# Kernel tuning notes

Measured on AMD Instinct MI355X. Metric: run time of the kernel, lower is better.

Reference implementation:

```python
import jax, jax.numpy as jnp
import numpy as np

STATE_DIM = 128
EDGE_DIM = 32
INNER_DIM = 256
B, N = 32, 128


def _lin_params(key, fan_in, fan_out):
    kw, kb = jax.random.split(key)
    bound = 1.0 / np.sqrt(fan_in)
    W = jax.random.uniform(kw, (fan_in, fan_out), minval=-bound, maxval=bound, dtype=jnp.float32)
    b = jax.random.uniform(kb, (fan_out,), minval=-bound, maxval=bound, dtype=jnp.float32)
    return W, b


def setup_inputs() -> dict:
    key = jax.random.key(0)
    ks = jax.random.split(key, 10)
    h = jax.random.normal(ks[0], (B, N, STATE_DIM), dtype=jnp.float32)
    edge_feat = jax.random.normal(ks[1], (B, N, N, EDGE_DIM), dtype=jnp.float32)
    edge_mask = jax.random.uniform(ks[2], (B, N, N), dtype=jnp.float32)
    in_dim = 2 * STATE_DIM + EDGE_DIM
    Wm1, bm1 = _lin_params(ks[3], in_dim, INNER_DIM)
    Wm2, bm2 = _lin_params(ks[4], INNER_DIM, STATE_DIM)
    Wg1, bg1 = _lin_params(ks[5], in_dim, INNER_DIM)
    Wg2, bg2 = _lin_params(ks[6], INNER_DIM, 1)
    Wu1, bu1 = _lin_params(ks[7], 2 * STATE_DIM + 1, INNER_DIM)
    Wu2, bu2 = _lin_params(ks[8], INNER_DIM, STATE_DIM)
    ln_w = jnp.ones((STATE_DIM,), jnp.float32)
    ln_b = jnp.zeros((STATE_DIM,), jnp.float32)
    return dict(h=h, edge_feat=edge_feat, edge_mask=edge_mask,
                Wm1=Wm1, bm1=bm1, Wm2=Wm2, bm2=bm2,
                Wg1=Wg1, bg1=bg1, Wg2=Wg2, bg2=bg2,
                Wu1=Wu1, bu1=bu1, Wu2=Wu2, bu2=bu2,
                ln_w=ln_w, ln_b=ln_b)


def _layernorm(x, w, b, eps=1e-5):
    mu = jnp.mean(x, axis=-1, keepdims=True)
    var = jnp.mean((x - mu) ** 2, axis=-1, keepdims=True)
    return (x - mu) * jax.lax.rsqrt(var + eps) * w + b


def reference(h, edge_feat, edge_mask,
              Wm1, bm1, Wm2, bm2,
              Wg1, bg1, Wg2, bg2,
              Wu1, bu1, Wu2, bu2,
              ln_w, ln_b):
    n = h.shape[1]
    # all-pairs concat [B,N,N,2*state+edge]; h_i broadcast over axis 2, h_j over axis 1
    h_i = jnp.broadcast_to(h[:, :, None, :], (h.shape[0], n, n, h.shape[-1]))
    h_j = jnp.broadcast_to(h[:, None, :, :], (h.shape[0], n, n, h.shape[-1]))
    pair = jnp.concatenate([h_i, h_j, edge_feat], axis=-1)
    gate = jax.nn.sigmoid(jnp.tanh(pair @ Wg1 + bg1) @ Wg2 + bg2) * edge_mask[..., None]
    msg = jnp.tanh(pair @ Wm1 + bm1) @ Wm2 + bm2
    denom = jnp.maximum(jnp.sum(gate, axis=2), 1.0)  # [B,N,1]
    agg = jnp.sum(gate * msg, axis=2) / denom  # [B,N,state]
    degree = jnp.sum(edge_mask, axis=-1, keepdims=True)
    degree_norm = degree / max(n - 1, 1)
    upd_in = jnp.concatenate([h, agg, degree_norm], axis=-1)
    delta = jnp.tanh(jnp.tanh(upd_in @ Wu1 + bu1) @ Wu2 + bu2)
    return _layernorm(h + delta, ln_w, ln_b)
```

## Files before the change

### kernel.cpp

```cpp
#include <hip/hip_runtime.h>
#include <hip/hip_bf16.h>

#define BB 32
#define NN 128
#define SD 128
#define ED 32
#define ID 256
#define BN (BB*NN)
#define NI 4

#define WM2B 288
#define WU1B 352
#define WU2B 480

typedef __attribute__((ext_vector_type(8))) short sh8;
typedef __attribute__((ext_vector_type(4))) float f32x4;

__device__ __forceinline__ float ftanh(float x) {
    float e2 = __expf(2.0f * x);
    return 1.0f - 2.0f * __builtin_amdgcn_rcpf(e2 + 1.0f);
}

__device__ __forceinline__ ushort f2bf(float f) {
    unsigned u = __float_as_uint(f);
    return (ushort)((u + 0x7FFF + ((u >> 16) & 1)) >> 16);
}

__device__ __forceinline__ sh8 afragT(const float* base, int stride, int kt, int lane) {
    sh8 v = (sh8){0, 0, 0, 0, 0, 0, 0, 0};
    if ((lane & 15) < 4) {
        const float* p = base + (lane & 15) * stride + kt * 32 + (lane >> 4) * 8;
        f32x4 a0 = *(const f32x4*)p;
        f32x4 a1 = *(const f32x4*)(p + 4);
        v[0] = (short)f2bf(a0[0]); v[1] = (short)f2bf(a0[1]);
        v[2] = (short)f2bf(a0[2]); v[3] = (short)f2bf(a0[3]);
        v[4] = (short)f2bf(a1[0]); v[5] = (short)f2bf(a1[1]);
        v[6] = (short)f2bf(a1[2]); v[7] = (short)f2bf(a1[3]);
    }
    return v;
}

__global__ void k_prep(const float* __restrict__ Wg1, const float* __restrict__ Wm1,
                       const float* __restrict__ Wm2, const float* __restrict__ Wu1,
                       const float* __restrict__ Wu2, ushort* __restrict__ Bprep) {
    const int tt = blockIdx.x;
    const int l = threadIdx.x;
    const float* W;
    int rowbase, nt, stride;
    if (tt < 256) {
        const int tgt = tt >> 6;
        const int kt = (tt >> 4) & 3;
        nt = tt & 15;
        W = (tgt >= 2) ? Wm1 : Wg1;
        rowbase = (tgt & 1) * 128 + kt * 32;
        stride = ID;
    } else if (tt < WM2B) {
        const int wt = tt - 256;
        W = (wt >> 4) ? Wm1 : Wg1;
        rowbase = 2 * SD;
        nt = wt & 15;
        stride = ID;
    } else if (tt < WU1B) {
        const int wt = tt - WM2B;
        W = Wm2; rowbase = (wt >> 3) * 32; nt = wt & 7; stride = SD;
    } else if (tt < WU2B) {
        const int wt = tt - WU1B;
        W = Wu1; rowbase = (wt >> 4) * 32; nt = wt & 15; stride = ID;
    } else {
        const int wt = tt - WU2B;
        W = Wu2; rowbase = (wt >> 3) * 32; nt = wt & 7; stride = SD;
    }
    const int colw = nt * 16 + (l & 15);
    const int kb = rowbase + (l >> 4) * 8;
    sh8 v;
    #pragma unroll
    for (int e = 0; e < 8; ++e)
        v[e] = (short)f2bf(W[(size_t)(kb + e) * stride + colw]);
    *(sh8*)&Bprep[(size_t)tt * 512 + l * 8] = v;
}

__global__ __launch_bounds__(256) void k1_mfma(
        const float* __restrict__ h,
        const float* __restrict__ bg1, const float* __restrict__ bm1,
        const ushort* __restrict__ Bprep,
        float* __restrict__ Hgi, float* __restrict__ Hgjt,
        float* __restrict__ Hmi, float* __restrict__ Hmjt) {
    const int blk = blockIdx.x;
    const int tgt = blockIdx.y;
    const int t = threadIdx.x;
    const int w = t >> 6;
    const int lane = t & 63;
    const int col = lane & 15;
    const int grp = lane >> 4;
    __shared__ __align__(16) ushort Alds[4 * 512];

    {
        const int c = t;
        const int kt = c >> 6, l = c & 63;
        const int row = l & 15;
        const int kb = kt * 32 + (l >> 4) * 8;
        const float* p = h + (size_t)(blk * 16 + row) * SD + kb;
        f32x4 a0 = *(const f32x4*)p;
        f32x4 a1 = *(const f32x4*)(p + 4);
        sh8 v;
        v[0] = (short)f2bf(a0[0]); v[1] = (short)f2bf(a0[1]);
        v[2] = (short)f2bf(a0[2]); v[3] = (short)f2bf(a0[3]);
        v[4] = (short)f2bf(a1[0]); v[5] = (short)f2bf(a1[1]);
        v[6] = (short)f2bf(a1[2]); v[7] = (short)f2bf(a1[3]);
        *(sh8*)&Alds[c * 8] = v;
    }
    __syncthreads();

    const int kcol = w * 64 + col;
    sh8 Af[4];
    #pragma unroll
    for (int kt = 0; kt < 4; ++kt)
        Af[kt] = *(const sh8*)&Alds[kt * 512 + lane * 8];

    f32x4 acc[4];
    #pragma unroll
    for (int n = 0; n < 4; ++n) acc[n] = (f32x4){0.f, 0.f, 0.f, 0.f};
    #pragma unroll
    for (int kt = 0; kt < 4; ++kt)
        #pragma unroll
        for (int n = 0; n < 4; ++n) {
            sh8 Bf = *(const sh8*)&Bprep[
                (size_t)(tgt * 64 + kt * 16 + w * 4 + n) * 512 + lane * 8];
            acc[n] = __builtin_amdgcn_mfma_f32_16x16x32_bf16(
                Af[kt], Bf, acc[n], 0, 0, 0);
        }
    if (tgt & 1) {
        float* out = (tgt == 1) ? Hgjt : Hmjt;
        #pragma unroll
        for (int n = 0; n < 4; ++n)
            *(f32x4*)&out[((size_t)blk * ID + kcol + n * 16) * 16 + grp * 4] = acc[n];
    } else {
        const float* bias = (tgt == 0) ? bg1 : bm1;
        float* out = (tgt == 0) ? Hgi : Hmi;
        #pragma unroll
        for (int n = 0; n < 4; ++n) {
            const float bv = bias[kcol + n * 16];
            #pragma unroll
            for (int r = 0; r < 4; ++r)
                out[(size_t)(blk * 16 + grp * 4 + r) * ID + kcol + n * 16] =
                    acc[n][r] + bv;
        }
    }
}

__global__ __launch_bounds__(256, 4) void k2_fused(
        const float* __restrict__ ef, const float* __restrict__ em,
        const ushort* __restrict__ Bprep,
        const float* __restrict__ Hgi, const float* __restrict__ Hmi,
        const float* __restrict__ Hgjt, const float* __restrict__ Hmjt,
        const float* __restrict__ Wg2, const float* __restrict__ bg2,
        const float* __restrict__ h,
        const float* __restrict__ Wu1, const float* __restrict__ bu1,
        const float* __restrict__ bu2, const float* __restrict__ bm2,
        const float* __restrict__ lnw, const float* __restrict__ lnb,
        float* __restrict__ out) {
    const int bi0 = blockIdx.x * NI;
    const int b = bi0 >> 7;
    const int t = threadIdx.x;
    const int w = t >> 6;
    const int lane = t & 63;
    const int col = lane & 15;
    const int grp = lane >> 4;

    __shared__ __align__(16) ushort Elds[NI * 4 * 512];
    __shared__ float glds[NI][NN];
    __shared__ float gsumL[NI], degL[NI];

    {
        float* gl = &glds[0][0];
        gl[t] = 0.f;
        gl[t + 256] = 0.f;
    }

    const int kcol = w * 64 + col;
    const float* HgjL = Hgjt + (size_t)b * 8 * ID * 16 + (size_t)kcol * 16 + grp * 4;
    const float* HmjL = Hmjt + (size_t)b * 8 * ID * 16 + (size_t)kcol * 16 + grp * 4;
    const float bg2v = bg2[0];

    float ts[NI][4];
    #pragma unroll
    for (int i = 0; i < NI; ++i)
        #pragma unroll
        for (int n = 0; n < 4; ++n) ts[i][n] = 0.f;
    float gs_run = 0.f, dv_run = 0.f;

    for (int half = 0; half < 2; ++half) {
        __syncthreads();
        #pragma unroll
        for (int i = 0; i < NI; ++i) {
            const float* efb = ef + (size_t)(bi0 + i) * NN * ED;
            const int c = t;
            const int j = (half * 4 + (c >> 6)) * 16 + (c & 15);
            const int kb = ((c >> 4) & 3) * 8;
            const float* p = efb + j * ED + kb;
            f32x4 a0 = *(const f32x4*)p;
            f32x4 a1 = *(const f32x4*)(p + 4);
            sh8 v;
            v[0] = (short)f2bf(a0[0]); v[1] = (short)f2bf(a0[1]);
            v[2] = (short)f2bf(a0[2]); v[3] = (short)f2bf(a0[3]);
            v[4] = (short)f2bf(a1[0]); v[5] = (short)f2bf(a1[1]);
            v[6] = (short)f2bf(a1[2]); v[7] = (short)f2bf(a1[3]);
            *(sh8*)&Elds[i * 2048 + c * 8] = v;
        }
        __syncthreads();

        {
            sh8 Bg[4];
            float hgiR[NI][4], wg2R[4];
            #pragma unroll
            for (int n = 0; n < 4; ++n) {
                Bg[n] = *(const sh8*)&Bprep[(size_t)(256 + w * 4 + n) * 512 + lane * 8];
                wg2R[n] = Wg2[kcol + n * 16];
            }
            #pragma unroll
            for (int i = 0; i < NI; ++i)
                #pragma unroll
                for (int n = 0; n < 4; ++n)
                    hgiR[i][n] = Hgi[(size_t)(bi0 + i) * ID + kcol + n * 16];
            const float* Hbase = HgjL + (size_t)(half * 4) * (ID * 16);
            f32x4 Cg[4], Cn[4];
            #pragma unroll
            for (int n = 0; n < 4; ++n) Cg[n] = *(const f32x4*)(Hbase + n * 256);
            for (int st = 0; st < 4; ++st) {
                if (st < 3) {
                    const float* ps = Hbase + (size_t)(st + 1) * (ID * 16);
                    #pragma unroll
                    for (int n = 0; n < 4; ++n) Cn[n] = *(const f32x4*)(ps + n * 256);
                }
                #pragma unroll
                for (int i = 0; i < NI; ++i) {
                    sh8 Af = *(const sh8*)&Elds[i * 2048 + st * 512 + lane * 8];
                    f32x4 acc[4];
                    #pragma unroll
                    for (int n = 0; n < 4; ++n)
                        acc[n] = __builtin_amdgcn_mfma_f32_16x16x32_bf16(
                            Af, Bg[n], Cg[n], 0, 0, 0);
                    float p[4] = {0.f, 0.f, 0.f, 0.f};
                    #pragma unroll
                    for (int n = 0; n < 4; ++n)
                        #pragma unroll
                        for (int r = 0; r < 4; ++r)
                            p[r] = fmaf(ftanh(acc[n][r] + hgiR[i][n]), wg2R[n], p[r]);
                    #pragma unroll
                    for (int m = 1; m < 16; m <<= 1)
                        #pragma unroll
                        for (int r = 0; r < 4; ++r) p[r] += __shfl_xor(p[r], m, 64);
                    if (col == 0) {
                        #pragma unroll
                        for (int r = 0; r < 4; ++r)
                            atomicAdd(&glds[i][(half * 4 + st) * 16 + grp * 4 + r],
                                      p[r]);
                    }
                }
                #pragma unroll
                for (int n = 0; n < 4; ++n) Cg[n] = Cn[n];
            }
        }
        __syncthreads();

        {
            const int j = half * 64 + lane;
            const float pre = glds[w][j] + bg2v;
            const float m = em[(size_t)(bi0 + w) * NN + j];
            const float g = m * __builtin_amdgcn_rcpf(1.0f + __expf(-pre));
            glds[w][j] = g;
            gs_run += g;
            dv_run += m;
        }
        __syncthreads();

        {
            sh8 Bm[4];
            float hmiR[NI][4];
            #pragma unroll
            for (int n = 0; n < 4; ++n)
                Bm[n] = *(const sh8*)&Bprep[(size_t)(272 + w * 4 + n) * 512 + lane * 8];
            #pragma unroll
            for (int i = 0; i < NI; ++i)
                #pragma unroll
                for (int n = 0; n < 4; ++n)
                    hmiR[i][n] = Hmi[(size_t)(bi0 + i) * ID + kcol + n * 16];
            const float* Hbase = HmjL + (size_t)(half * 4) * (ID * 16);
            f32x4 Cm[4], Cn[4];
            #pragma unroll
            for (int n = 0; n < 4; ++n) Cm[n] = *(const f32x4*)(Hbase + n * 256);
            for (int st = 0; st < 4; ++st) {
                if (st < 3) {
                    const float* ps = Hbase + (size_t)(st + 1) * (ID * 16);
                    #pragma unroll
                    for (int n = 0; n < 4; ++n) Cn[n] = *(const f32x4*)(ps + n * 256);
                }
                #pragma unroll
                for (int i = 0; i < NI; ++i) {
                    sh8 Af = *(const sh8*)&Elds[i * 2048 + st * 512 + lane * 8];
                    f32x4 acc[4];
                    #pragma unroll
                    for (int n = 0; n < 4; ++n)
                        acc[n] = __builtin_amdgcn_mfma_f32_16x16x32_bf16(
                            Af, Bm[n], Cm[n], 0, 0, 0);
                    f32x4 gr = *(const f32x4*)&glds[i][(half * 4 + st) * 16 + grp * 4];
                    #pragma unroll
                    for (int n = 0; n < 4; ++n)
                        #pragma unroll
                        for (int r = 0; r < 4; ++r)
                            ts[i][n] = fmaf(gr[r], ftanh(acc[n][r] + hmiR[i][n]),
                                            ts[i][n]);
                }
                #pragma unroll
                for (int n = 0; n < 4; ++n) Cm[n] = Cn[n];
            }
        }
    }

    #pragma unroll
    for (int mm = 1; mm < 64; mm <<= 1) {
        gs_run += __shfl_xor(gs_run, mm, 64);
        dv_run += __shfl_xor(dv_run, mm, 64);
    }
    if (lane == 0) { gsumL[w] = gs_run; degL[w] = dv_run; }

    #pragma unroll
    for (int i = 0; i < NI; ++i)
        #pragma unroll
        for (int n = 0; n < 4; ++n) {
            ts[i][n] += __shfl_xor(ts[i][n], 16, 64);
            ts[i][n] += __shfl_xor(ts[i][n], 32, 64);
        }

    __syncthreads();
    float* scratch = (float*)Elds;
    float* Tl  = scratch;
    float* up  = scratch + 1024;
    float* uu  = scratch + 2064;
    float* xsb = scratch + 3088;
    if (lane < 16) {
        #pragma unroll
        for (int i = 0; i < NI; ++i)
            #pragma unroll
            for (int n = 0; n < 4; ++n)
                Tl[i * 256 + w * 64 + n * 16 + lane] = ts[i][n];
    }
    #pragma unroll
    for (int it = 0; it < 2; ++it) {
        const int idx = it * 256 + t;
        const int i = idx >> 7, c = idx & 127;
        up[i * 260 + c] = h[(size_t)(bi0 + i) * SD + c];
    }
    if (t < NI) up[t * 260 + 256] = degL[t] * (1.0f / 127.0f);
    __syncthreads();

    {
        f32x4 acc[2];
        acc[0] = (f32x4){0.f, 0.f, 0.f, 0.f};
        acc[1] = (f32x4){0.f, 0.f, 0.f, 0.f};
        #pragma unroll
        for (int kt = 0; kt < 8; ++kt) {
            sh8 Af = afragT(Tl, 256, kt, lane);
            #pragma unroll
            for (int n2 = 0; n2 < 2; ++n2) {
                sh8 Bf = *(const sh8*)&Bprep[
                    (size_t)(WM2B + kt * 8 + w * 2 + n2) * 512 + lane * 8];
                acc[n2] = __builtin_amdgcn_mfma_f32_16x16x32_bf16(Af, Bf, acc[n2], 0, 0, 0);
            }
        }
        if (grp == 0) {
            #pragma unroll
            for (int n2 = 0; n2 < 2; ++n2) {
                const int d = (w * 2 + n2) * 16 + lane;
                const float bmv = bm2[d];
                #pragma unroll
                for (int r = 0; r < 4; ++r) {
                    const float g = gsumL[r];
                    up[r * 260 + SD + d] = fmaf(g, bmv, acc[n2][r]) *
                                           __builtin_amdgcn_rcpf(fmaxf(g, 1.0f));
                }
            }
        }
    }
    __syncthreads();

    {
        f32x4 acc[4];
        #pragma unroll
        for (int n2 = 0; n2 < 4; ++n2) acc[n2] = (f32x4){0.f, 0.f, 0.f, 0.f};
        #pragma unroll
        for (int kt = 0; kt < 8; ++kt) {
            sh8 Af = afragT(up, 260, kt, lane);
            #pragma unroll
            for (int n2 = 0; n2 < 4; ++n2) {
                sh8 Bf = *(const sh8*)&Bprep[
                    (size_t)(WU1B + kt * 16 + w * 4 + n2) * 512 + lane * 8];
                acc[n2] = __builtin_amdgcn_mfma_f32_16x16x32_bf16(Af, Bf, acc[n2], 0, 0, 0);
            }
        }
        if (grp == 0) {
            #pragma unroll
            for (int n2 = 0; n2 < 4; ++n2) {
                const int kc = (w * 4 + n2) * 16 + lane;
                const float wdeg = Wu1[(size_t)(2 * SD) * ID + kc];
                const float bb = bu1[kc];
                #pragma unroll
                for (int r = 0; r < 4; ++r)
                    uu[r * 256 + kc] =
                        ftanh(acc[n2][r] + bb + up[r * 260 + 256] * wdeg);
            }
        }
    }
    __syncthreads();

    {
        f32x4 acc[2];
        acc[0] = (f32x4){0.f, 0.f, 0.f, 0.f};
        acc[1] = (f32x4){0.f, 0.f, 0.f, 0.f};
        #pragma unroll
        for (int kt = 0; kt < 8; ++kt) {
            sh8 Af = afragT(uu, 256, kt, lane);
            #pragma unroll
            for (int n2 = 0; n2 < 2; ++n2) {
                sh8 Bf = *(const sh8*)&Bprep[
                    (size_t)(WU2B + kt * 8 + w * 2 + n2) * 512 + lane * 8];
                acc[n2] = __builtin_amdgcn_mfma_f32_16x16x32_bf16(Af, Bf, acc[n2], 0, 0, 0);
            }
        }
        if (grp == 0) {
            #pragma unroll
            for (int n2 = 0; n2 < 2; ++n2) {
                const int d = (w * 2 + n2) * 16 + lane;
                const float bb = bu2[d];
                #pragma unroll
                for (int r = 0; r < 4; ++r)
                    xsb[r * 128 + d] = up[r * 260 + d] + ftanh(acc[n2][r] + bb);
            }
        }
    }
    __syncthreads();

    {
        const float v0 = xsb[w * 128 + lane], v1 = xsb[w * 128 + lane + 64];
        float s = v0 + v1;
        #pragma unroll
        for (int m = 1; m < 64; m <<= 1) s += __shfl_xor(s, m, 64);
        const float mu = s * (1.0f / SD);
        const float d0 = v0 - mu, d1 = v1 - mu;
        float q = d0 * d0 + d1 * d1;
        #pragma unroll
        for (int m = 1; m < 64; m <<= 1) q += __shfl_xor(q, m, 64);
        const float inv = rsqrtf(q * (1.0f / SD) + 1e-5f);
        out[(size_t)(bi0 + w) * SD + lane] = d0 * inv * lnw[lane] + lnb[lane];
        out[(size_t)(bi0 + w) * SD + lane + 64] =
            d1 * inv * lnw[lane + 64] + lnb[lane + 64];
    }
}

extern "C" void kernel_launch(void* const* d_in, const int* in_sizes, int n_in,
                              void* d_out, int out_size, void* d_ws, size_t ws_size,
                              hipStream_t stream) {
    const float* h   = (const float*)d_in[0];
    const float* ef  = (const float*)d_in[1];
    const float* em  = (const float*)d_in[2];
    const float* Wm1 = (const float*)d_in[3];
    const float* bm1 = (const float*)d_in[4];
    const float* Wm2 = (const float*)d_in[5];
    const float* bm2 = (const float*)d_in[6];
    const float* Wg1 = (const float*)d_in[7];
    const float* bg1 = (const float*)d_in[8];
    const float* Wg2 = (const float*)d_in[9];
    const float* bg2 = (const float*)d_in[10];
    const float* Wu1 = (const float*)d_in[11];
    const float* bu1 = (const float*)d_in[12];
    const float* Wu2 = (const float*)d_in[13];
    const float* bu2 = (const float*)d_in[14];
    const float* lnw = (const float*)d_in[15];
    const float* lnb = (const float*)d_in[16];

    float* ws = (float*)d_ws;
    float* Hgi   = ws;
    float* Hgjt  = Hgi + (size_t)BN * ID;
    float* Hmi   = Hgjt + (size_t)BN * ID;
    float* Hmjt  = Hmi + (size_t)BN * ID;
    ushort* Bprep = (ushort*)(Hmjt + (size_t)BN * ID);
    float* outp = (float*)d_out;

    k_prep<<<544, 64, 0, stream>>>(Wg1, Wm1, Wm2, Wu1, Wu2, Bprep);
    k1_mfma<<<dim3(BN / 16, 4), 256, 0, stream>>>(h, bg1, bm1, Bprep,
                                                  Hgi, Hgjt, Hmi, Hmjt);
    k2_fused<<<BN / NI, 256, 0, stream>>>(ef, em, Bprep, Hgi, Hmi, Hgjt, Hmjt,
                                          Wg2, bg2, h, Wu1, bu1, bu2, bm2,
                                          lnw, lnb, outp);
}
```

Baseline: 149.9 us.

## Split gate and message passes into separate loops over halves

Restructures the per-half loop so that all gate MFMA work for both halves runs first, then a single sigmoid/mask pass computes gates and row sums with wave reductions, then a second loop reloads edge features and runs the message MFMAs. This cuts the number of barriers between gate and message phases and keeps fewer registers live at once, since ts accumulators no longer coexist with the gate working set. The cost is converting and staging the edge features into LDS twice per half.

```diff
diff --git a/kernel.cpp b/kernel.cpp
--- a/kernel.cpp
+++ b/kernel.cpp
@@ -169,6 +169,7 @@
 
     __shared__ __align__(16) ushort Elds[NI * 4 * 512];
     __shared__ float glds[NI][NN];
+    __shared__ float red[2][4][2];
     __shared__ float gsumL[NI], degL[NI];
 
     {
@@ -180,14 +181,6 @@
     const int kcol = w * 64 + col;
     const float* HgjL = Hgjt + (size_t)b * 8 * ID * 16 + (size_t)kcol * 16 + grp * 4;
     const float* HmjL = Hmjt + (size_t)b * 8 * ID * 16 + (size_t)kcol * 16 + grp * 4;
-    const float bg2v = bg2[0];
-
-    float ts[NI][4];
-    #pragma unroll
-    for (int i = 0; i < NI; ++i)
-        #pragma unroll
-        for (int n = 0; n < 4; ++n) ts[i][n] = 0.f;
-    float gs_run = 0.f, dv_run = 0.f;
 
     for (int half = 0; half < 2; ++half) {
         __syncthreads();
@@ -209,121 +202,150 @@
         }
         __syncthreads();
 
-        {
-            sh8 Bg[4];
-            float hgiR[NI][4], wg2R[4];
-            #pragma unroll
-            for (int n = 0; n < 4; ++n) {
-                Bg[n] = *(const sh8*)&Bprep[(size_t)(256 + w * 4 + n) * 512 + lane * 8];
-                wg2R[n] = Wg2[kcol + n * 16];
-            }
-            #pragma unroll
-            for (int i = 0; i < NI; ++i)
+        sh8 Bg[4];
+        float hgiR[NI][4], wg2R[4];
+        #pragma unroll
+        for (int n = 0; n < 4; ++n) {
+            Bg[n] = *(const sh8*)&Bprep[(size_t)(256 + w * 4 + n) * 512 + lane * 8];
+            wg2R[n] = Wg2[kcol + n * 16];
+        }
+        #pragma unroll
+        for (int i = 0; i < NI; ++i)
+            #pragma unroll
+            for (int n = 0; n < 4; ++n)
+                hgiR[i][n] = Hgi[(size_t)(bi0 + i) * ID + kcol + n * 16];
+        const float* Hbase = HgjL + (size_t)(half * 4) * (ID * 16);
+        f32x4 Cg[4], Cn[4];
+        #pragma unroll
+        for (int n = 0; n < 4; ++n) Cg[n] = *(const f32x4*)(Hbase + n * 256);
+        for (int st = 0; st < 4; ++st) {
+            if (st < 3) {
+                const float* ps = Hbase + (size_t)(st + 1) * (ID * 16);
+                #pragma unroll
+                for (int n = 0; n < 4; ++n) Cn[n] = *(const f32x4*)(ps + n * 256);
+            }
+            #pragma unroll
+            for (int i = 0; i < NI; ++i) {
+                sh8 Af = *(const sh8*)&Elds[i * 2048 + st * 512 + lane * 8];
+                f32x4 acc[4];
                 #pragma unroll
                 for (int n = 0; n < 4; ++n)
-                    hgiR[i][n] = Hgi[(size_t)(bi0 + i) * ID + kcol + n * 16];
-            const float* Hbase = HgjL + (size_t)(half * 4) * (ID * 16);
-            f32x4 Cg[4], Cn[4];
-            #pragma unroll
-            for (int n = 0; n < 4; ++n) Cg[n] = *(const f32x4*)(Hbase + n * 256);
-            for (int st = 0; st < 4; ++st) {
-                if (st < 3) {
-                    const float* ps = Hbase + (size_t)(st + 1) * (ID * 16);
+                    acc[n] = __builtin_amdgcn_mfma_f32_16x16x32_bf16(
+                        Af, Bg[n], Cg[n], 0, 0, 0);
+                float p[4] = {0.f, 0.f, 0.f, 0.f};
+                #pragma unroll
+                for (int n = 0; n < 4; ++n)
                     #pragma unroll
-                    for (int n = 0; n < 4; ++n) Cn[n] = *(const f32x4*)(ps + n * 256);
+                    for (int r = 0; r < 4; ++r)
+                        p[r] = fmaf(ftanh(acc[n][r] + hgiR[i][n]), wg2R[n], p[r]);
+                #pragma unroll
+                for (int m = 1; m < 16; m <<= 1)
+                    #pragma unroll
+                    for (int r = 0; r < 4; ++r) p[r] += __shfl_xor(p[r], m, 64);
+                if (col == 0) {
+                    #pragma unroll
+                    for (int r = 0; r < 4; ++r)
+                        atomicAdd(&glds[i][(half * 4 + st) * 16 + grp * 4 + r],
+                                  p[r]);
                 }
-                #pragma unroll
-                for (int i = 0; i < NI; ++i) {
-                    sh8 Af = *(const sh8*)&Elds[i * 2048 + st * 512 + lane * 8];
-                    f32x4 acc[4];
+            }
+            #pragma unroll
+            for (int n = 0; n < 4; ++n) Cg[n] = Cn[n];
+        }
+    }
+    __syncthreads();
+
+    {
+        const float bg2v = bg2[0];
+        #pragma unroll
+        for (int it = 0; it < NI / 2; ++it) {
+            const int i = it * 2 + (t >> 7);
+            const int j = t & 127;
+            const float pre = glds[i][j] + bg2v;
+            const float m = em[(size_t)(bi0 + i) * NN + j];
+            const float g = m * __builtin_amdgcn_rcpf(1.0f + __expf(-pre));
+            glds[i][j] = g;
+            float gsv = g, dv = m;
+            #pragma unroll
+            for (int mm = 1; mm < 64; mm <<= 1) {
+                gsv += __shfl_xor(gsv, mm, 64);
+                dv  += __shfl_xor(dv, mm, 64);
+            }
+            if (lane == 0) { red[it][w][0] = gsv; red[it][w][1] = dv; }
+        }
+    }
+    __syncthreads();
+    if (t < NI) {
+        const int it = t >> 1, w0 = (t & 1) * 2;
+        gsumL[t] = red[it][w0][0] + red[it][w0 + 1][0];
+        degL[t]  = red[it][w0][1] + red[it][w0 + 1][1];
+    }
+
+    float ts[NI][4];
+    #pragma unroll
+    for (int i = 0; i < NI; ++i)
+        #pragma unroll
+        for (int n = 0; n < 4; ++n) ts[i][n] = 0.f;
+    for (int half = 0; half < 2; ++half) {
+        __syncthreads();
+        #pragma unroll
+        for (int i = 0; i < NI; ++i) {
+            const float* efb = ef + (size_t)(bi0 + i) * NN * ED;
+            const int c = t;
+            const int j = (half * 4 + (c >> 6)) * 16 + (c & 15);
+            const int kb = ((c >> 4) & 3) * 8;
+            const float* p = efb + j * ED + kb;
+            f32x4 a0 = *(const f32x4*)p;
+            f32x4 a1 = *(const f32x4*)(p + 4);
+            sh8 v;
+            v[0] = (short)f2bf(a0[0]); v[1] = (short)f2bf(a0[1]);
+            v[2] = (short)f2bf(a0[2]); v[3] = (short)f2bf(a0[3]);
+            v[4] = (short)f2bf(a1[0]); v[5] = (short)f2bf(a1[1]);
+            v[6] = (short)f2bf(a1[2]); v[7] = (short)f2bf(a1[3]);
+            *(sh8*)&Elds[i * 2048 + c * 8] = v;
+        }
+        __syncthreads();
+
+        sh8 Bm[4];
+        float hmiR[NI][4];
+        #pragma unroll
+        for (int n = 0; n < 4; ++n)
+            Bm[n] = *(const sh8*)&Bprep[(size_t)(272 + w * 4 + n) * 512 + lane * 8];
+        #pragma unroll
+        for (int i = 0; i < NI; ++i)
+            #pragma unroll
+            for (int n = 0; n < 4; ++n)
+                hmiR[i][n] = Hmi[(size_t)(bi0 + i) * ID + kcol + n * 16];
+        const float* Hbase = HmjL + (size_t)(half * 4) * (ID * 16);
+        f32x4 Cm[4], Cn[4];
+        #pragma unroll
+        for (int n = 0; n < 4; ++n) Cm[n] = *(const f32x4*)(Hbase + n * 256);
+        for (int st = 0; st < 4; ++st) {
+            if (st < 3) {
+                const float* ps = Hbase + (size_t)(st + 1) * (ID * 16);
+                #pragma unroll
+                for (int n = 0; n < 4; ++n) Cn[n] = *(const f32x4*)(ps + n * 256);
+            }
+            #pragma unroll
+            for (int i = 0; i < NI; ++i) {
+                sh8 Af = *(const sh8*)&Elds[i * 2048 + st * 512 + lane * 8];
+                f32x4 acc[4];
+                #pragma unroll
+                for (int n = 0; n < 4; ++n)
+                    acc[n] = __builtin_amdgcn_mfma_f32_16x16x32_bf16(
+                        Af, Bm[n], Cm[n], 0, 0, 0);
+                f32x4 gr = *(const f32x4*)&glds[i][(half * 4 + st) * 16 + grp * 4];
+                #pragma unroll
+                for (int n = 0; n < 4; ++n)
                     #pragma unroll
-                    for (int n = 0; n < 4; ++n)
-                        acc[n] = __builtin_amdgcn_mfma_f32_16x16x32_bf16(
-                            Af, Bg[n], Cg[n], 0, 0, 0);
-                    float p[4] = {0.f, 0.f, 0.f, 0.f};
-                    #pragma unroll
-                    for (int n = 0; n < 4; ++n)
-                        #pragma unroll
-                        for (int r = 0; r < 4; ++r)
-                            p[r] = fmaf(ftanh(acc[n][r] + hgiR[i][n]), wg2R[n], p[r]);
-                    #pragma unroll
-                    for (int m = 1; m < 16; m <<= 1)
-                        #pragma unroll
-                        for (int r = 0; r < 4; ++r) p[r] += __shfl_xor(p[r], m, 64);
-                    if (col == 0) {
-                        #pragma unroll
-                        for (int r = 0; r < 4; ++r)
-                            atomicAdd(&glds[i][(half * 4 + st) * 16 + grp * 4 + r],
-                                      p[r]);
-                    }
-                }
-                #pragma unroll
-                for (int n = 0; n < 4; ++n) Cg[n] = Cn[n];
-            }
-        }
-        __syncthreads();
-
-        {
-            const int j = half * 64 + lane;
-            const float pre = glds[w][j] + bg2v;
-            const float m = em[(size_t)(bi0 + w) * NN + j];
-            const float g = m * __builtin_amdgcn_rcpf(1.0f + __expf(-pre));
-            glds[w][j] = g;
-            gs_run += g;
-            dv_run += m;
-        }
-        __syncthreads();
-
-        {
-            sh8 Bm[4];
-            float hmiR[NI][4];
-            #pragma unroll
-            for (int n = 0; n < 4; ++n)
-                Bm[n] = *(const sh8*)&Bprep[(size_t)(272 + w * 4 + n) * 512 + lane * 8];
-            #pragma unroll
-            for (int i = 0; i < NI; ++i)
-                #pragma unroll
-                for (int n = 0; n < 4; ++n)
-                    hmiR[i][n] = Hmi[(size_t)(bi0 + i) * ID + kcol + n * 16];
-            const float* Hbase = HmjL + (size_t)(half * 4) * (ID * 16);
-            f32x4 Cm[4], Cn[4];
-            #pragma unroll
-            for (int n = 0; n < 4; ++n) Cm[n] = *(const f32x4*)(Hbase + n * 256);
-            for (int st = 0; st < 4; ++st) {
-                if (st < 3) {
-                    const float* ps = Hbase + (size_t)(st + 1) * (ID * 16);
-                    #pragma unroll
-                    for (int n = 0; n < 4; ++n) Cn[n] = *(const f32x4*)(ps + n * 256);
-                }
-                #pragma unroll
-                for (int i = 0; i < NI; ++i) {
-                    sh8 Af = *(const sh8*)&Elds[i * 2048 + st * 512 + lane * 8];
-                    f32x4 acc[4];
-                    #pragma unroll
-                    for (int n = 0; n < 4; ++n)
-                        acc[n] = __builtin_amdgcn_mfma_f32_16x16x32_bf16(
-                            Af, Bm[n], Cm[n], 0, 0, 0);
-                    f32x4 gr = *(const f32x4*)&glds[i][(half * 4 + st) * 16 + grp * 4];
-                    #pragma unroll
-                    for (int n = 0; n < 4; ++n)
-                        #pragma unroll
-                        for (int r = 0; r < 4; ++r)
-                            ts[i][n] = fmaf(gr[r], ftanh(acc[n][r] + hmiR[i][n]),
-                                            ts[i][n]);
-                }
-                #pragma unroll
-                for (int n = 0; n < 4; ++n) Cm[n] = Cn[n];
-            }
-        }
-    }
-
-    #pragma unroll
-    for (int mm = 1; mm < 64; mm <<= 1) {
-        gs_run += __shfl_xor(gs_run, mm, 64);
-        dv_run += __shfl_xor(dv_run, mm, 64);
-    }
-    if (lane == 0) { gsumL[w] = gs_run; degL[w] = dv_run; }
-
+                    for (int r = 0; r < 4; ++r)
+                        ts[i][n] = fmaf(gr[r], ftanh(acc[n][r] + hmiR[i][n]),
+                                        ts[i][n]);
+            }
+            #pragma unroll
+            for (int n = 0; n < 4; ++n) Cm[n] = Cn[n];
+        }
+    }
     #pragma unroll
     for (int i = 0; i < NI; ++i)
         #pragma unroll
```

Measured after the change: 124.0 us. 17.3% less time.
